# Kernel optimization log

Hardware: AMD Instinct MI355X
Metric: run time of the kernel (lower is better)

## Reference

```python
import jax, jax.numpy as jnp
import numpy as np

NUM_BUCKETS = 320
MAX_DISTANCE = 800


def _layer_norm(x, w, b, eps=1e-5):
    x32 = x.astype(jnp.float32)
    mu = x32.mean(-1, keepdims=True)
    var = x32.var(-1, keepdims=True)
    return ((x32 - mu) / jnp.sqrt(var + eps) * w + b).astype(x.dtype)


def _rel_pos_bucket(rel):
    half = NUM_BUCKETS // 2            # 160
    st = half // 2                     # 80 (small threshold)
    sign = (rel >= 0).astype(jnp.int32)
    ab = jnp.abs(rel)
    is_small = ab < st
    log_ratio = jnp.log(jnp.clip(ab.astype(jnp.float32), 1.0) / st) / np.float32(np.log(MAX_DISTANCE / st))
    log_pos = st + (log_ratio * (half - st)).astype(jnp.int32)  # trunc toward zero like .long()
    log_pos = jnp.minimum(log_pos, half - 1)
    bucket = jnp.where(is_small, ab, log_pos) + sign * half
    return jnp.clip(bucket, 0, NUM_BUCKETS - 1)


def setup_inputs() -> dict:
    key = jax.random.key(0)
    B, T, C, H, FF = 2, 2048, 768, 12, 3072
    D = C // H
    ks = jax.random.split(key, 16)
    s = 0.02
    return {
        "x": jax.random.normal(ks[0], (B, T, C), jnp.float32),
        "ln1_w": jnp.ones((C,), jnp.float32),
        "ln1_b": jnp.zeros((C,), jnp.float32),
        "wq": jax.random.normal(ks[1], (C, C), jnp.float32) * s,
        "bq": jnp.zeros((C,), jnp.float32),
        "wk": jax.random.normal(ks[2], (C, C), jnp.float32) * s,
        "bk": jnp.zeros((C,), jnp.float32),
        "wv": jax.random.normal(ks[3], (C, C), jnp.float32) * s,
        "bv": jnp.zeros((C,), jnp.float32),
        "wo": jax.random.normal(ks[4], (C, C), jnp.float32) * s,
        "bo": jnp.zeros((C,), jnp.float32),
        "ln2_w": jnp.ones((C,), jnp.float32),
        "ln2_b": jnp.zeros((C,), jnp.float32),
        "w1": jax.random.normal(ks[5], (FF, C), jnp.float32) * s,
        "b1": jnp.zeros((FF,), jnp.float32),
        "w2": jax.random.normal(ks[6], (C, FF), jnp.float32) * s,
        "b2": jnp.zeros((C,), jnp.float32),
        "rel_embed": jax.random.normal(ks[7], (NUM_BUCKETS, H), jnp.float32),
        "gate_ur_w": jax.random.normal(ks[8], (H, D), jnp.float32) * 0.01,
        "gate_i_w": jax.random.normal(ks[9], (H, D), jnp.float32) * 0.01,
        "rel_scale": jnp.ones((H,), jnp.float32),
    }


def reference(x, ln1_w, ln1_b, wq, bq, wk, bk, wv, bv, wo, bo,
              ln2_w, ln2_b, w1, b1, w2, b2, rel_embed, gate_ur_w, gate_i_w, rel_scale):
    B, T, C = x.shape
    H = rel_embed.shape[1]
    D = C // H

    residual = x
    h = _layer_norm(x, ln1_w, ln1_b)
    q = (h @ wq.T + bq).reshape(B, T, H, D).transpose(0, 2, 1, 3)  # [B,H,T,D]
    k = (h @ wk.T + bk).reshape(B, T, H, D).transpose(0, 2, 1, 3)
    v = (h @ wv.T + bv).reshape(B, T, H, D).transpose(0, 2, 1, 3)

    attn = jnp.einsum('bhqd,bhkd->bhqk', q, k) * (D ** -0.5)

    # gated relative position bias
    pos = jnp.arange(T)
    rel = pos[None, :] - pos[:, None]                 # [T,T]
    buckets = _rel_pos_bucket(rel)                    # [T,T]
    pe = rel_embed[buckets]                           # [T,T,H]
    pe = jnp.transpose(pe, (2, 0, 1))[None]           # [1,H,T,T]
    g_in = q.mean(axis=2).transpose(0, 2, 1).mean(axis=-1)   # [B,D]
    gate_r = jax.nn.sigmoid(g_in @ gate_ur_w.T)       # [B,H]
    gate_u = jax.nn.sigmoid(g_in @ gate_i_w.T)        # [B,H]
    gate = 1.0 + (gate_u * rel_scale[None, :] * gate_r)[:, :, None, None]
    bias = pe * gate                                  # [B,H,T,T]

    attn = jax.nn.softmax(attn + bias, axis=-1)
    out = jnp.einsum('bhqk,bhkd->bhqd', attn, v).transpose(0, 2, 1, 3).reshape(B, T, C)
    x = residual + out @ wo.T + bo

    residual = x
    h = _layer_norm(x, ln2_w, ln2_b)
    h = jax.nn.gelu(h @ w1.T + b1, approximate=False) @ w2.T + b2
    return residual + h
```

## Files before the change

### kernel.cpp

```cpp
#include <hip/hip_runtime.h>
#include <hip/hip_bf16.h>


#define Tn 2048
#define Cn 768
#define Hn 12
#define Dn 64
#define FFn 3072
#define Mn 4096
#define QKVS 2304
#define LQK 1536

typedef __attribute__((ext_vector_type(8))) short bfrag;
typedef __attribute__((ext_vector_type(8))) unsigned short us8;
typedef __attribute__((ext_vector_type(4))) float f32x4;

#define GLDS(gptr, lptr) __builtin_amdgcn_global_load_lds( \
    (const __attribute__((address_space(1))) void*)(gptr), \
    (__attribute__((address_space(3))) void*)(lptr), 16, 0, 0)

__device__ __forceinline__ unsigned short f2bu(float f){
  __hip_bfloat16 h = __float2bfloat16(f);
  return *(unsigned short*)&h;
}
__device__ __forceinline__ float bu2f(unsigned short u){
  union { unsigned int i; float f; } v; v.i = ((unsigned int)u) << 16; return v.f;
}
__device__ __forceinline__ us8 pack8(float4 a, float4 b){
  us8 c;
  c[0]=f2bu(a.x); c[1]=f2bu(a.y); c[2]=f2bu(a.z); c[3]=f2bu(a.w);
  c[4]=f2bu(b.x); c[5]=f2bu(b.y); c[6]=f2bu(b.z); c[7]=f2bu(b.w);
  return c;
}
__device__ __forceinline__ float fexp2(float x){ return __builtin_amdgcn_exp2f(x); }

__device__ __forceinline__ float block_reduce_sum(float v, float* sred){
  #pragma unroll
  for (int off = 32; off > 0; off >>= 1) v += __shfl_down(v, off, 64);
  __syncthreads();
  if ((threadIdx.x & 63) == 0) sred[threadIdx.x >> 6] = v;
  __syncthreads();
  return sred[0] + sred[1] + sred[2] + sred[3];
}

__global__ __launch_bounds__(256) void cast_all_kernel(
    const float* __restrict__ wq, const float* __restrict__ wk,
    const float* __restrict__ wv, const float* __restrict__ wo,
    const float* __restrict__ w1, const float* __restrict__ w2,
    const float* __restrict__ bq, const float* __restrict__ bk,
    const float* __restrict__ bv, const float* __restrict__ rel_embed,
    unsigned short* __restrict__ Wqkv, unsigned short* __restrict__ Wob,
    unsigned short* __restrict__ W1b, unsigned short* __restrict__ W2b,
    float* __restrict__ bias_rel, float* __restrict__ bqkv)
{
  const int blk = blockIdx.x;
  if (blk >= 3472){
    const int i = (blk - 3472) * 256 + threadIdx.x;
    bqkv[i] = (i < Cn) ? bq[i] : (i < 2 * Cn) ? bk[i - Cn] : bv[i - 2 * Cn];
    return;
  }
  if (blk >= 3456){
    const int idx = (blk - 3456) * 256 + threadIdx.x;
    if (idx >= 4095) return;
    const int rel = idx - 2047;
    const int ab = rel < 0 ? -rel : rel;
    int bucket;
    if (ab < 80){
      bucket = ab;
    } else {
      const float lr = logf((float)ab * (1.0f / 80.0f)) * (1.0f / 2.3025851f);
      int lp = 80 + (int)(lr * 80.0f);
      bucket = lp < 159 ? lp : 159;
    }
    if (rel >= 0) bucket += 160;
    #pragma unroll
    for (int h = 0; h < Hn; h++)
      bias_rel[h * 4095 + idx] = rel_embed[bucket * Hn + h] * 1.44269504089f;
    return;
  }
  const float* src; unsigned short* dst; int i;
  if (blk < 288)      { src = wq; dst = Wqkv;               i = blk * 256 + threadIdx.x; }
  else if (blk < 576) { src = wk; dst = Wqkv + Cn * Cn;     i = (blk - 288) * 256 + threadIdx.x; }
  else if (blk < 864) { src = wv; dst = Wqkv + 2 * Cn * Cn; i = (blk - 576) * 256 + threadIdx.x; }
  else if (blk < 1152){ src = wo; dst = Wob;                i = (blk - 864) * 256 + threadIdx.x; }
  else if (blk < 2304){ src = w1; dst = W1b;                i = (blk - 1152) * 256 + threadIdx.x; }
  else                { src = w2; dst = W2b;                i = (blk - 2304) * 256 + threadIdx.x; }
  const float4 a = ((const float4*)src)[i * 2];
  const float4 b = ((const float4*)src)[i * 2 + 1];
  *(us8*)&dst[i * 8] = pack8(a, b);
}

__global__ __launch_bounds__(256) void ln_kernel(const float* __restrict__ xin,
    const float* __restrict__ w, const float* __restrict__ bsh,
    unsigned short* __restrict__ out)
{
  __shared__ float xs[Cn];
  __shared__ float sred[4];
  const size_t base = (size_t)blockIdx.x * Cn;
  float s = 0.f;
  for (int c = threadIdx.x; c < Cn; c += 256){
    float v = xin[base + c];
    xs[c] = v; s += v;
  }
  const float mean = block_reduce_sum(s, sred) * (1.f / Cn);
  float s2 = 0.f;
  for (int c = threadIdx.x; c < Cn; c += 256){
    float d = xs[c] - mean; s2 += d * d;
  }
  const float var = block_reduce_sum(s2, sred) * (1.f / Cn);
  const float rstd = rsqrtf(var + 1e-5f);
  for (int c = threadIdx.x; c < Cn; c += 256)
    out[base + c] = f2bu((xs[c] - mean) * rstd * w[c] + bsh[c]);
}

template<int EPI, bool TRANSV>
__global__ __launch_bounds__(256) void gemm_mfma_kernel(
    const unsigned short* __restrict__ A, const unsigned short* __restrict__ Bw,
    const float* __restrict__ bias, unsigned short* __restrict__ vt,
    void* __restrict__ Cout, int M, int N, int K, int ldo)
{
  __shared__ __align__(16) unsigned short As[128 * 32];
  __shared__ __align__(16) unsigned short Bs[128 * 32];
  const int tid = threadIdx.x;
  const int lane = tid & 63, w = tid >> 6;
  const int nl = lane & 15, quad = lane >> 4;
  const int wm = w >> 1, wn = w & 1;
  const int id = blockIdx.x;
  const int bm = ((id & 7) * 4 + ((id >> 3) & 3)) * 128;
  const int bn = (id >> 5) * 128;
  const int l4 = lane >> 2, lk = (lane & 3) * 8;

  f32x4 acc[4][4];
  #pragma unroll
  for (int i = 0; i < 4; i++)
    #pragma unroll
    for (int j = 0; j < 4; j++) acc[i][j] = (f32x4){0.f, 0.f, 0.f, 0.f};

  const int c0 = w, c1 = w + 4;
  const unsigned short* A0 = A + (size_t)(bm + c0 * 16 + l4) * K + lk;
  const unsigned short* A1 = A + (size_t)(bm + c1 * 16 + l4) * K + lk;
  const unsigned short* B0 = Bw + (size_t)(bn + c0 * 16 + l4) * K + lk;
  const unsigned short* B1 = Bw + (size_t)(bn + c1 * 16 + l4) * K + lk;

  for (int k0 = 0; k0 < K; k0 += 32){
    __syncthreads();
    GLDS(A0 + k0, &As[c0 * 512]); GLDS(A1 + k0, &As[c1 * 512]);
    GLDS(B0 + k0, &Bs[c0 * 512]); GLDS(B1 + k0, &Bs[c1 * 512]);
    __syncthreads();
    bfrag Af[4], Bf[4];
    #pragma unroll
    for (int mt = 0; mt < 4; mt++)
      Af[mt] = *(const bfrag*)&As[(wm * 64 + mt * 16 + nl) * 32 + quad * 8];
    #pragma unroll
    for (int nt = 0; nt < 4; nt++)
      Bf[nt] = *(const bfrag*)&Bs[(wn * 64 + nt * 16 + nl) * 32 + quad * 8];
    #pragma unroll
    for (int mt = 0; mt < 4; mt++)
      #pragma unroll
      for (int nt = 0; nt < 4; nt++)
        acc[mt][nt] = __builtin_amdgcn_mfma_f32_16x16x32_bf16(Af[mt], Bf[nt], acc[mt][nt], 0, 0, 0);
  }

  if (TRANSV && bn >= 1536){
    #pragma unroll
    for (int nt = 0; nt < 4; nt++){
      const int col = bn + wn * 64 + nt * 16 + nl;
      const float bv_ = bias[col];
      const int vcol = col - 1536;
      #pragma unroll
      for (int mt = 0; mt < 4; mt++){
        const int row0 = bm + wm * 64 + mt * 16 + quad * 4;
        unsigned short pk[4];
        #pragma unroll
        for (int r = 0; r < 4; r++) pk[r] = f2bu(acc[mt][nt][r] + bv_);
        *(uint2*)&vt[(size_t)vcol * Mn + row0] = *(uint2*)pk;
      }
    }
    return;
  }
  #pragma unroll
  for (int nt = 0; nt < 4; nt++){
    const int col = bn + wn * 64 + nt * 16 + nl;
    const float bv_ = bias[col];
    #pragma unroll
    for (int mt = 0; mt < 4; mt++){
      const int row0 = bm + wm * 64 + mt * 16 + quad * 4;
      #pragma unroll
      for (int r = 0; r < 4; r++){
        const size_t idx = (size_t)(row0 + r) * ldo + col;
        const float v = acc[mt][nt][r] + bv_;
        if (EPI == 2){
          ((unsigned short*)Cout)[idx] = f2bu(0.5f * v * (1.f + erff(v * 0.70710678118f)));
        } else {
          ((unsigned short*)Cout)[idx] = f2bu(v);
        }
      }
    }
  }
}

__global__ __launch_bounds__(256) void gemm_t64_kernel(
    const unsigned short* __restrict__ A, const unsigned short* __restrict__ Bw,
    const float* __restrict__ bias, const float* __restrict__ res,
    float* __restrict__ Cout, int M, int N, int K)
{
  __shared__ __align__(16) unsigned short As[64 * 32];
  __shared__ __align__(16) unsigned short Bs[64 * 32];
  const int tid = threadIdx.x;
  const int lane = tid & 63, w = tid >> 6;
  const int nl = lane & 15, quad = lane >> 4;
  const int id = blockIdx.x;
  const int bm = ((id & 7) * 8 + ((id >> 3) & 7)) * 64;
  const int bn = (id >> 6) * 64;
  const int l4 = lane >> 2, lk = (lane & 3) * 8;

  f32x4 acc[4];
  #pragma unroll
  for (int j = 0; j < 4; j++) acc[j] = (f32x4){0.f, 0.f, 0.f, 0.f};

  const unsigned short* A0 = A + (size_t)(bm + w * 16 + l4) * K + lk;
  const unsigned short* B0 = Bw + (size_t)(bn + w * 16 + l4) * K + lk;

  for (int k0 = 0; k0 < K; k0 += 32){
    __syncthreads();
    GLDS(A0 + k0, &As[w * 512]);
    GLDS(B0 + k0, &Bs[w * 512]);
    __syncthreads();
    const bfrag Af = *(const bfrag*)&As[(w * 16 + nl) * 32 + quad * 8];
    bfrag Bf[4];
    #pragma unroll
    for (int nt = 0; nt < 4; nt++)
      Bf[nt] = *(const bfrag*)&Bs[(nt * 16 + nl) * 32 + quad * 8];
    #pragma unroll
    for (int nt = 0; nt < 4; nt++)
      acc[nt] = __builtin_amdgcn_mfma_f32_16x16x32_bf16(Af, Bf[nt], acc[nt], 0, 0, 0);
  }

  const int row0 = bm + w * 16 + quad * 4;
  #pragma unroll
  for (int nt = 0; nt < 4; nt++){
    const int col = bn + nt * 16 + nl;
    const float bv_ = bias[col];
    #pragma unroll
    for (int r = 0; r < 4; r++){
      const size_t idx = (size_t)(row0 + r) * N + col;
      Cout[idx] = acc[nt][r] + bv_ + res[idx];
    }
  }
}

__global__ __launch_bounds__(256) void qmean_part_kernel(
    const unsigned short* __restrict__ QKVqk, float* __restrict__ qpart)
{
  __shared__ float ps[Cn];
  const int b = blockIdx.y, t0 = blockIdx.x * 128;
  const int tid = threadIdx.x;
  float a0 = 0.f, a1 = 0.f, a2 = 0.f;
  for (int r = 0; r < 128; r++){
    const size_t base = (size_t)(b * Tn + t0 + r) * LQK;
    a0 += bu2f(QKVqk[base + tid]);
    a1 += bu2f(QKVqk[base + tid + 256]);
    a2 += bu2f(QKVqk[base + tid + 512]);
  }
  ps[tid] = a0; ps[tid + 256] = a1; ps[tid + 512] = a2;
  __syncthreads();
  if (tid < Dn){
    float s = 0.f;
    #pragma unroll
    for (int hh = 0; hh < Hn; hh++) s += ps[hh * Dn + tid];
    qpart[(b * 16 + blockIdx.x) * Dn + tid] = s;
  }
}

__global__ __launch_bounds__(64) void gate_kernel(const float* __restrict__ qpart,
    const float* __restrict__ gur, const float* __restrict__ gi,
    const float* __restrict__ rsc, float* __restrict__ gate)
{
  const int b = blockIdx.x / Hn, h = blockIdx.x % Hn;
  const int d = threadIdx.x;
  float s = 0.f;
  #pragma unroll
  for (int blk = 0; blk < 16; blk++) s += qpart[(b * 16 + blk) * Dn + d];
  const float g = s * (1.f / (Hn * Tn));
  float vr = g * gur[h * Dn + d];
  float vu = g * gi[h * Dn + d];
  #pragma unroll
  for (int off = 32; off > 0; off >>= 1){
    vr += __shfl_down(vr, off, 64);
    vu += __shfl_down(vu, off, 64);
  }
  if (d == 0){
    const float gr = 1.f / (1.f + __expf(-vr));
    const float gu = 1.f / (1.f + __expf(-vu));
    gate[blockIdx.x] = 1.f + gu * rsc[h] * gr;
  }
}

__global__ __launch_bounds__(256) void attn_mfma_kernel(
    const unsigned short* __restrict__ QKVqk, const unsigned short* __restrict__ VT,
    const float* __restrict__ bias_rel, const float* __restrict__ gate,
    unsigned short* __restrict__ O)
{
  __shared__ __align__(16) char smem[9216 * 4 + 1024];
  unsigned short* Qs = (unsigned short*)smem;
  float* bias_blk    = (float*)smem;
  unsigned short* Ks = (unsigned short*)(smem + 9216);
  unsigned short* Vt = (unsigned short*)(smem + 18432);
  unsigned short* Ptq = (unsigned short*)(smem + 27648);
  float* lsh         = (float*)(smem + 36864);

  const int qbase = blockIdx.x * 64;
  const int h = blockIdx.y, b = blockIdx.z;
  const int tid = threadIdx.x;
  const float g = gate[b * Hn + h];
  const float* brow = bias_rel + h * 4095 + 1984 - qbase;
  const unsigned short* Q = QKVqk;
  const unsigned short* K = QKVqk + Cn;

  {
    const int row = tid >> 2, cg = (tid & 3) * 16;
    const us8* qp = (const us8*)(Q + (size_t)(b * Tn + qbase + row) * LQK + h * Dn + cg);
    *(us8*)&Qs[row * 72 + cg]     = qp[0];
    *(us8*)&Qs[row * 72 + cg + 8] = qp[1];
  }
  __syncthreads();

  const int lane = tid & 63, w = tid >> 6;
  const int nl = lane & 15, quad = lane >> 4;

  bfrag Qb[4][2];
  #pragma unroll
  for (int mt = 0; mt < 4; mt++){
    Qb[mt][0] = *(const bfrag*)&Qs[(mt * 16 + nl) * 72 + quad * 8];
    Qb[mt][1] = *(const bfrag*)&Qs[(mt * 16 + nl) * 72 + 32 + quad * 8];
  }
  __syncthreads();
  for (int j = tid; j < 2111; j += 256) bias_blk[j] = brow[j] * g;

  const int wq = w & 1, wd = w >> 1;
  f32x4 Oa[2][2];
  #pragma unroll
  for (int a = 0; a < 2; a++)
    #pragma unroll
    for (int d0 = 0; d0 < 2; d0++) Oa[a][d0] = (f32x4){0.f, 0.f, 0.f, 0.f};
  float l_part[4] = {0.f, 0.f, 0.f, 0.f};

  const int skey = tid >> 2, sdg = (tid & 3) * 16;
  const int vd = tid >> 3, vk8 = (tid & 7) * 8;
  const unsigned short* vtg = VT + (size_t)(h * Dn) * Mn + (size_t)b * Tn;

  for (int kt = 0; kt < 32; kt++){
    const int kbase = kt * 64;
    __syncthreads();
    {
      const us8* kp = (const us8*)(K + (size_t)(b * Tn + kbase + skey) * LQK + h * Dn + sdg);
      *(us8*)&Ks[skey * 72 + sdg]     = kp[0];
      *(us8*)&Ks[skey * 72 + sdg + 8] = kp[1];
    }
    {
      const us8 v0 = *(const us8*)&vtg[(size_t)vd * Mn + kbase + vk8];
      const us8 v1 = *(const us8*)&vtg[(size_t)(32 + vd) * Mn + kbase + vk8];
      *(us8*)&Vt[vd * 72 + vk8]        = v0;
      *(us8*)&Vt[(32 + vd) * 72 + vk8] = v1;
    }
    __syncthreads();

    const bfrag Ka0 = *(const bfrag*)&Ks[(w * 16 + nl) * 72 + quad * 8];
    const bfrag Ka1 = *(const bfrag*)&Ks[(w * 16 + nl) * 72 + 32 + quad * 8];
    const int bofs = kbase + w * 16 + quad * 4 + 63 - nl;
    #pragma unroll
    for (int mt = 0; mt < 4; mt++){
      f32x4 z = (f32x4){0.f, 0.f, 0.f, 0.f};
      z = __builtin_amdgcn_mfma_f32_16x16x32_bf16(Ka0, Qb[mt][0], z, 0, 0, 0);
      z = __builtin_amdgcn_mfma_f32_16x16x32_bf16(Ka1, Qb[mt][1], z, 0, 0, 0);
      unsigned short pk[4];
      #pragma unroll
      for (int r = 0; r < 4; r++){
        const float p = fexp2(z[r] * 0.18033688f + bias_blk[bofs - mt * 16 + r]);
        l_part[mt] += p;
        pk[r] = f2bu(p);
      }
      *(uint2*)&Ptq[(mt * 16 + nl) * 72 + w * 16 + quad * 4] = *(uint2*)pk;
    }
    __syncthreads();

    bfrag Vf[2][2], Pf[2][2];
    #pragma unroll
    for (int d0 = 0; d0 < 2; d0++){
      const int dt = wd * 2 + d0;
      Vf[d0][0] = *(const bfrag*)&Vt[(dt * 16 + nl) * 72 + quad * 8];
      Vf[d0][1] = *(const bfrag*)&Vt[(dt * 16 + nl) * 72 + 32 + quad * 8];
    }
    #pragma unroll
    for (int a = 0; a < 2; a++){
      const int qt = wq * 2 + a;
      Pf[a][0] = *(const bfrag*)&Ptq[(qt * 16 + nl) * 72 + quad * 8];
      Pf[a][1] = *(const bfrag*)&Ptq[(qt * 16 + nl) * 72 + 32 + quad * 8];
    }
    #pragma unroll
    for (int a = 0; a < 2; a++)
      #pragma unroll
      for (int d0 = 0; d0 < 2; d0++){
        Oa[a][d0] = __builtin_amdgcn_mfma_f32_16x16x32_bf16(Vf[d0][0], Pf[a][0], Oa[a][d0], 0, 0, 0);
        Oa[a][d0] = __builtin_amdgcn_mfma_f32_16x16x32_bf16(Vf[d0][1], Pf[a][1], Oa[a][d0], 0, 0, 0);
      }
  }

  #pragma unroll
  for (int mt = 0; mt < 4; mt++){
    float l = l_part[mt];
    l += __shfl_xor(l, 16, 64);
    l += __shfl_xor(l, 32, 64);
    if (quad == 0) lsh[w * 64 + mt * 16 + nl] = l;
  }
  __syncthreads();
  #pragma unroll
  for (int a = 0; a < 2; a++){
    const int q = (wq * 2 + a) * 16 + nl;
    const float linv = 1.f / (lsh[q] + lsh[64 + q] + lsh[128 + q] + lsh[192 + q]);
    unsigned short* orow = O + (size_t)(b * Tn + qbase + q) * Cn + h * Dn;
    #pragma unroll
    for (int d0 = 0; d0 < 2; d0++){
      unsigned short pk[4];
      #pragma unroll
      for (int r = 0; r < 4; r++) pk[r] = f2bu(Oa[a][d0][r] * linv);
      *(uint2*)&orow[(wd * 2 + d0) * 16 + quad * 4] = *(uint2*)pk;
    }
  }
}

extern "C" void kernel_launch(void* const* d_in, const int* in_sizes, int n_in,
                              void* d_out, int out_size, void* d_ws, size_t ws_size,
                              hipStream_t stream)
{
  const float* x     = (const float*)d_in[0];
  const float* ln1_w = (const float*)d_in[1];
  const float* ln1_b = (const float*)d_in[2];
  const float* wq    = (const float*)d_in[3];
  const float* bq    = (const float*)d_in[4];
  const float* wk    = (const float*)d_in[5];
  const float* bk    = (const float*)d_in[6];
  const float* wv    = (const float*)d_in[7];
  const float* bv    = (const float*)d_in[8];
  const float* wo    = (const float*)d_in[9];
  const float* bo    = (const float*)d_in[10];
  const float* ln2_w = (const float*)d_in[11];
  const float* ln2_b = (const float*)d_in[12];
  const float* w1    = (const float*)d_in[13];
  const float* b1    = (const float*)d_in[14];
  const float* w2    = (const float*)d_in[15];
  const float* b2    = (const float*)d_in[16];
  const float* rel_embed = (const float*)d_in[17];
  const float* gur   = (const float*)d_in[18];
  const float* gi    = (const float*)d_in[19];
  const float* rsc   = (const float*)d_in[20];

  char* ws = (char*)d_ws;
  unsigned short* QKVqk = (unsigned short*)(ws);
  unsigned short* VT    = (unsigned short*)(ws + 12582912);
  unsigned short* Ob    = (unsigned short*)(ws + 18874368);
  float*          X2    = (float*)(ws + 25165824);
  unsigned short* Hb    = (unsigned short*)(ws + 37748736);
  unsigned short* Wqkv  = (unsigned short*)(ws + 44040192);
  unsigned short* Wob   = (unsigned short*)(ws + 47579136);
  unsigned short* W1b   = (unsigned short*)(ws + 48758784);
  unsigned short* W2b   = (unsigned short*)(ws + 53477376);
  float*          bqkv  = (float*)(ws + 58195968);
  float*          bias_rel = (float*)(ws + 58205184);
  float*          qpart = (float*)(ws + 58401744);
  float*          gate  = (float*)(ws + 58409936);
  unsigned short* Fb    = (unsigned short*)(ws);

  cast_all_kernel<<<3481, 256, 0, stream>>>(wq, wk, wv, wo, w1, w2, bq, bk, bv,
                                            rel_embed, Wqkv, Wob, W1b, W2b,
                                            bias_rel, bqkv);
  ln_kernel<<<Mn, 256, 0, stream>>>(x, ln1_w, ln1_b, Hb);
  gemm_mfma_kernel<0, true><<<(QKVS / 128) * (Mn / 128), 256, 0, stream>>>(
      Hb, Wqkv, bqkv, VT, QKVqk, Mn, QKVS, Cn, LQK);
  qmean_part_kernel<<<dim3(16, 2), 256, 0, stream>>>(QKVqk, qpart);
  gate_kernel<<<2 * Hn, 64, 0, stream>>>(qpart, gur, gi, rsc, gate);
  attn_mfma_kernel<<<dim3(Tn / 64, Hn, 2), 256, 0, stream>>>(QKVqk, VT, bias_rel, gate, Ob);
  gemm_t64_kernel<<<(Cn / 64) * (Mn / 64), 256, 0, stream>>>(
      Ob, Wob, bo, x, X2, Mn, Cn, Cn);
  ln_kernel<<<Mn, 256, 0, stream>>>(X2, ln2_w, ln2_b, Hb);
  gemm_mfma_kernel<2, false><<<(FFn / 128) * (Mn / 128), 256, 0, stream>>>(
      Hb, W1b, b1, nullptr, Fb, Mn, FFn, Cn, FFn);
  gemm_t64_kernel<<<(Cn / 64) * (Mn / 64), 256, 0, stream>>>(
      Fb, W2b, b2, X2, (float*)d_out, Mn, Cn, FFn);
}
```

Measured before the change: 340.7 us.

## Double-buffer attention K/V tiles via async LDS loads and widen GEMM K-step

The attention kernel now prefetches the next 64-key K and V^T tiles into a second LDS buffer with global_load_lds while the current tile is computed. This removes the register-staged copy and one barrier per iteration, so global latency can overlap with MFMA and exp work. The residual GEMM now loads two 32-wide K slices per iteration, halving its barrier count. Costs are more LDS per block, which can lower occupancy, and unpadded 32-element rows that may cause LDS bank conflicts.

```diff
diff --git a/kernel.cpp b/kernel.cpp
--- a/kernel.cpp
+++ b/kernel.cpp
@@ -204,36 +204,43 @@
     const float* __restrict__ bias, const float* __restrict__ res,
     float* __restrict__ Cout, int M, int N, int K)
 {
-  __shared__ __align__(16) unsigned short As[64 * 32];
-  __shared__ __align__(16) unsigned short Bs[64 * 32];
+  __shared__ __align__(16) unsigned short As[2 * 64 * 32];
+  __shared__ __align__(16) unsigned short Bs[2 * 64 * 32];
   const int tid = threadIdx.x;
   const int lane = tid & 63, w = tid >> 6;
   const int nl = lane & 15, quad = lane >> 4;
   const int id = blockIdx.x;
   const int bm = ((id & 7) * 8 + ((id >> 3) & 7)) * 64;
   const int bn = (id >> 6) * 64;
-  const int l4 = lane >> 2, lk = (lane & 3) * 8;
+  const int l2 = lane >> 2, l3 = (lane & 3) * 8;
 
   f32x4 acc[4];
   #pragma unroll
   for (int j = 0; j < 4; j++) acc[j] = (f32x4){0.f, 0.f, 0.f, 0.f};
 
-  const unsigned short* A0 = A + (size_t)(bm + w * 16 + l4) * K + lk;
-  const unsigned short* B0 = Bw + (size_t)(bn + w * 16 + l4) * K + lk;
-
-  for (int k0 = 0; k0 < K; k0 += 32){
+  const unsigned short* A0 = A + (size_t)(bm + w * 16 + l2) * K + l3;
+  const unsigned short* B0 = Bw + (size_t)(bn + w * 16 + l2) * K + l3;
+
+  for (int k0 = 0; k0 < K; k0 += 64){
     __syncthreads();
-    GLDS(A0 + k0, &As[w * 512]);
-    GLDS(B0 + k0, &Bs[w * 512]);
+    GLDS(A0 + k0,      &As[w * 512]);
+    GLDS(A0 + k0 + 32, &As[2048 + w * 512]);
+    GLDS(B0 + k0,      &Bs[w * 512]);
+    GLDS(B0 + k0 + 32, &Bs[2048 + w * 512]);
     __syncthreads();
-    const bfrag Af = *(const bfrag*)&As[(w * 16 + nl) * 32 + quad * 8];
-    bfrag Bf[4];
-    #pragma unroll
-    for (int nt = 0; nt < 4; nt++)
-      Bf[nt] = *(const bfrag*)&Bs[(nt * 16 + nl) * 32 + quad * 8];
-    #pragma unroll
-    for (int nt = 0; nt < 4; nt++)
-      acc[nt] = __builtin_amdgcn_mfma_f32_16x16x32_bf16(Af, Bf[nt], acc[nt], 0, 0, 0);
+    const bfrag Af0 = *(const bfrag*)&As[(w * 16 + nl) * 32 + quad * 8];
+    const bfrag Af1 = *(const bfrag*)&As[2048 + (w * 16 + nl) * 32 + quad * 8];
+    bfrag Bf0[4], Bf1[4];
+    #pragma unroll
+    for (int nt = 0; nt < 4; nt++){
+      Bf0[nt] = *(const bfrag*)&Bs[(nt * 16 + nl) * 32 + quad * 8];
+      Bf1[nt] = *(const bfrag*)&Bs[2048 + (nt * 16 + nl) * 32 + quad * 8];
+    }
+    #pragma unroll
+    for (int nt = 0; nt < 4; nt++){
+      acc[nt] = __builtin_amdgcn_mfma_f32_16x16x32_bf16(Af0, Bf0[nt], acc[nt], 0, 0, 0);
+      acc[nt] = __builtin_amdgcn_mfma_f32_16x16x32_bf16(Af1, Bf1[nt], acc[nt], 0, 0, 0);
+    }
   }
 
   const int row0 = bm + w * 16 + quad * 4;
@@ -301,13 +308,13 @@
     const float* __restrict__ bias_rel, const float* __restrict__ gate,
     unsigned short* __restrict__ O)
 {
-  __shared__ __align__(16) char smem[9216 * 4 + 1024];
+  __shared__ __align__(16) char smem[52224];
   unsigned short* Qs = (unsigned short*)smem;
   float* bias_blk    = (float*)smem;
-  unsigned short* Ks = (unsigned short*)(smem + 9216);
-  unsigned short* Vt = (unsigned short*)(smem + 18432);
-  unsigned short* Ptq = (unsigned short*)(smem + 27648);
-  float* lsh         = (float*)(smem + 36864);
+  unsigned short* KsP = (unsigned short*)(smem + 9216);
+  unsigned short* VtP = (unsigned short*)(smem + 25600);
+  unsigned short* Ptq = (unsigned short*)(smem + 41984);
+  float* lsh         = (float*)(smem + 51200);
 
   const int qbase = blockIdx.x * 64;
   const int h = blockIdx.y, b = blockIdx.z;
@@ -317,6 +324,18 @@
   const unsigned short* Q = QKVqk;
   const unsigned short* K = QKVqk + Cn;
 
+  const int lane = tid & 63, w = tid >> 6;
+  const int nl = lane & 15, quad = lane >> 4;
+  const int l2 = lane >> 2, l3 = (lane & 3) * 8;
+
+  const unsigned short* kg0 = K + (size_t)(b * Tn + w * 16 + l2) * LQK + h * Dn + l3;
+  const unsigned short* vg0 = VT + (size_t)(h * Dn + w * 16 + l2) * Mn + (size_t)b * Tn + l3;
+
+  GLDS(kg0,      KsP + w * 512);
+  GLDS(kg0 + 32, KsP + 2048 + w * 512);
+  GLDS(vg0,      VtP + w * 512);
+  GLDS(vg0 + 32, VtP + 2048 + w * 512);
+
   {
     const int row = tid >> 2, cg = (tid & 3) * 16;
     const us8* qp = (const us8*)(Q + (size_t)(b * Tn + qbase + row) * LQK + h * Dn + cg);
@@ -325,9 +344,6 @@
   }
   __syncthreads();
 
-  const int lane = tid & 63, w = tid >> 6;
-  const int nl = lane & 15, quad = lane >> 4;
-
   bfrag Qb[4][2];
   #pragma unroll
   for (int mt = 0; mt < 4; mt++){
@@ -345,28 +361,22 @@
     for (int d0 = 0; d0 < 2; d0++) Oa[a][d0] = (f32x4){0.f, 0.f, 0.f, 0.f};
   float l_part[4] = {0.f, 0.f, 0.f, 0.f};
 
-  const int skey = tid >> 2, sdg = (tid & 3) * 16;
-  const int vd = tid >> 3, vk8 = (tid & 7) * 8;
-  const unsigned short* vtg = VT + (size_t)(h * Dn) * Mn + (size_t)b * Tn;
-
   for (int kt = 0; kt < 32; kt++){
     const int kbase = kt * 64;
+    const int cur = (kt & 1) * 4096;
+    const int nxt = 4096 - cur;
     __syncthreads();
-    {
-      const us8* kp = (const us8*)(K + (size_t)(b * Tn + kbase + skey) * LQK + h * Dn + sdg);
-      *(us8*)&Ks[skey * 72 + sdg]     = kp[0];
-      *(us8*)&Ks[skey * 72 + sdg + 8] = kp[1];
-    }
-    {
-      const us8 v0 = *(const us8*)&vtg[(size_t)vd * Mn + kbase + vk8];
-      const us8 v1 = *(const us8*)&vtg[(size_t)(32 + vd) * Mn + kbase + vk8];
-      *(us8*)&Vt[vd * 72 + vk8]        = v0;
-      *(us8*)&Vt[(32 + vd) * 72 + vk8] = v1;
-    }
-    __syncthreads();
-
-    const bfrag Ka0 = *(const bfrag*)&Ks[(w * 16 + nl) * 72 + quad * 8];
-    const bfrag Ka1 = *(const bfrag*)&Ks[(w * 16 + nl) * 72 + 32 + quad * 8];
+    if (kt < 31){
+      const unsigned short* kg = kg0 + (size_t)(kbase + 64) * LQK;
+      const unsigned short* vg = vg0 + kbase + 64;
+      GLDS(kg,      KsP + nxt + w * 512);
+      GLDS(kg + 32, KsP + nxt + 2048 + w * 512);
+      GLDS(vg,      VtP + nxt + w * 512);
+      GLDS(vg + 32, VtP + nxt + 2048 + w * 512);
+    }
+
+    const bfrag Ka0 = *(const bfrag*)&KsP[cur + (w * 16 + nl) * 32 + quad * 8];
+    const bfrag Ka1 = *(const bfrag*)&KsP[cur + 2048 + (w * 16 + nl) * 32 + quad * 8];
     const int bofs = kbase + w * 16 + quad * 4 + 63 - nl;
     #pragma unroll
     for (int mt = 0; mt < 4; mt++){
@@ -388,8 +398,8 @@
     #pragma unroll
     for (int d0 = 0; d0 < 2; d0++){
       const int dt = wd * 2 + d0;
-      Vf[d0][0] = *(const bfrag*)&Vt[(dt * 16 + nl) * 72 + quad * 8];
-      Vf[d0][1] = *(const bfrag*)&Vt[(dt * 16 + nl) * 72 + 32 + quad * 8];
+      Vf[d0][0] = *(const bfrag*)&VtP[cur + (dt * 16 + nl) * 32 + quad * 8];
+      Vf[d0][1] = *(const bfrag*)&VtP[cur + 2048 + (dt * 16 + nl) * 32 + quad * 8];
     }
     #pragma unroll
     for (int a = 0; a < 2; a++){
```

After: 329.6 us. -3.3%, faster.
